# Kernel optimization log

Hardware: AMD Instinct MI355X
Metric: run time of the kernel (lower is better)

The kernel has to match this reference:

```python
import jax, jax.numpy as jnp
import numpy as np

N, E, HID, H, D = 16000, 128000, 128, 8, 16
EPS = 1e-6
LN_EPS = 1e-5


def _ln(x, g, b):
    mu = x.mean(-1, keepdims=True)
    var = ((x - mu) ** 2).mean(-1, keepdims=True)
    return (x - mu) * jax.lax.rsqrt(var + LN_EPS) * g + b


def _phi(x):
    return jax.nn.elu(x) + 1.0


def setup_inputs() -> dict:
    key = jax.random.key(0)
    ks = jax.random.split(key, 16)
    w = lambda k, s: (jax.random.normal(k, s, jnp.float32) * 0.02)
    inp = {
        'x': jax.random.normal(ks[0], (N, HID), jnp.float32),
        'r': jax.random.normal(ks[1], (E, HID), jnp.float32),
        'edge_index': jax.random.randint(ks[2], (2, E), 0, N, jnp.int64),
        # layernorms
        'ln_x_g': jnp.ones((HID,)), 'ln_x_b': jnp.zeros((HID,)),
        'ln_r_g': jnp.ones((HID,)), 'ln_r_b': jnp.zeros((HID,)),
        'ln_post_g': jnp.ones((HID,)), 'ln_post_b': jnp.zeros((HID,)),
        'ln_ffpre_g': jnp.ones((HID,)), 'ln_ffpre_b': jnp.zeros((HID,)),
        'ln_ffpost_g': jnp.ones((HID,)), 'ln_ffpost_b': jnp.zeros((HID,)),
        # attention projections (stored [in, out]; y = x @ W)
        'Wq': w(ks[3], (HID, H * D)), 'Wk': w(ks[4], (HID, H * D)),
        'Wv': w(ks[5], (HID, H * D)),
        'Wkr': w(ks[6], (HID, H * D)), 'Wvr': w(ks[7], (HID, H * D)),
        'Wo': w(ks[8], (H * D, HID)),
        'Wg': w(ks[9], (2 * HID, HID)), 'bg': jnp.zeros((HID,)),
        'Ws': w(ks[10], (HID, HID)), 'bs': jnp.zeros((HID,)),
        # feed-forward
        'W1': w(ks[11], (HID, 4 * HID)), 'b1': jnp.zeros((4 * HID,)),
        'W2': w(ks[12], (4 * HID, HID)), 'b2': jnp.zeros((HID,)),
    }
    return inp


def reference(x, r, edge_index, ln_x_g, ln_x_b, ln_r_g, ln_r_b,
              ln_post_g, ln_post_b, ln_ffpre_g, ln_ffpre_b,
              ln_ffpost_g, ln_ffpost_b, Wq, Wk, Wv, Wkr, Wvr, Wo,
              Wg, bg, Ws, bs, W1, b1, W2, b2):
    n = x.shape[0]
    src, dst = edge_index[0], edge_index[1]
    xs = _ln(x, ln_x_g, ln_x_b)            # shared pre-norm (non-bipartite)
    rn = _ln(r, ln_r_g, ln_r_b)

    q = (xs @ Wq).reshape(n, H, D)
    k = (xs @ Wk).reshape(n, H, D)
    v = (xs @ Wv).reshape(n, H, D)
    k_e = k[src] + (rn @ Wkr).reshape(-1, H, D)   # [E,H,D]
    v_e = v[src] + (rn @ Wvr).reshape(-1, H, D)

    phi_q = _phi(q)                         # [N,H,D]
    phi_k = _phi(k_e)                       # [E,H,D]
    # per-edge outer product, scattered to destination nodes
    kv = phi_k[..., :, None] * v_e[..., None, :]          # [E,H,D,D]
    S = jax.ops.segment_sum(kv.reshape(-1, H * D * D), dst,
                            num_segments=n).reshape(n, H, D, D)
    Z = jax.ops.segment_sum(phi_k.reshape(-1, H * D), dst,
                            num_segments=n).reshape(n, H, D)

    num = jnp.einsum('nhd,nhdv->nhv', phi_q, S)
    den = jnp.maximum((phi_q * Z).sum(-1, keepdims=True), EPS)
    out = (num / den).reshape(n, H * D) @ Wo              # [N,HID]

    g = jax.nn.sigmoid(jnp.concatenate([out, xs], axis=-1) @ Wg + bg)
    attn = out + g * (xs @ Ws + bs - out)

    x_mid = x + _ln(attn, ln_post_g, ln_post_b)
    h = jax.nn.gelu(_ln(x_mid, ln_ffpre_g, ln_ffpre_b) @ W1 + b1,
                    approximate=False) @ W2 + b2
    return x_mid + _ln(h, ln_ffpost_g, ln_ffpost_b)
```

## Files before the change

kernel.cpp:

```cpp
#include <hip/hip_runtime.h>
#include <hip/hip_bf16.h>

#define NN 16000
#define NE 128000

typedef unsigned short u16;
typedef __attribute__((ext_vector_type(8))) short bf16x8;
typedef __attribute__((ext_vector_type(4))) float f32x4;

__device__ __forceinline__ float bf2f(u16 u) {
    unsigned int v = ((unsigned int)u) << 16;
    return __uint_as_float(v);
}
__device__ __forceinline__ u16 f2bf(float f) {
    unsigned int u = __float_as_uint(f);
    unsigned int r = u + 0x7FFF + ((u >> 16) & 1);
    return (u16)(r >> 16);
}
__device__ __forceinline__ float loadf(const void* p, size_t i, int bf) {
    return bf ? bf2f(((const u16*)p)[i]) : ((const float*)p)[i];
}

__device__ __forceinline__ int detect_bf(const u16* __restrict__ xw) {
    int lane = threadIdx.x & 63;
    int c = 0;
    #pragma unroll
    for (int k = 0; k < 16; ++k) {
        unsigned int w = xw[lane * 16 + k];
        int e = (int)((w >> 7) & 0xFF);
        c += (e >= 100 && e <= 140) ? 1 : 0;
    }
    for (int m = 1; m < 64; m <<= 1) c += __shfl_xor(c, m, 64);
    return c >= 850;
}

__device__ __forceinline__ int detect_e64(const int* __restrict__ ei) {
    int lane = threadIdx.x & 63;
    int a = 0;
    #pragma unroll
    for (int k = 0; k < 16; ++k) a |= ei[2 * (lane * 16 + k) + 1];
    for (int m = 1; m < 64; m <<= 1) a |= __shfl_xor(a, m, 64);
    return a == 0;
}

struct WDesc { const void* w; u16* wt; int K; int N; int off; int tile0; };
struct WTArgs { WDesc d[11]; };
__global__ __launch_bounds__(256) void pre1_kernel(const int* __restrict__ ei,
                                                   int* __restrict__ e32,
                                                   int* __restrict__ hist,
                                                   const u16* __restrict__ xw,
                                                   WTArgs args)
{
    int b = blockIdx.x;
    int tid = threadIdx.x;
    if (b < 250) {
        int e64 = detect_e64(ei);
        #pragma unroll
        for (int j = 0; j < 4; ++j) {
            int i = b * 1024 + j * 256 + tid;
            int v = e64 ? ei[2 * i] : ei[i];
            v = v < 0 ? 0 : (v >= NN ? NN - 1 : v);
            e32[i] = v;
            if (i >= NE) atomicAdd(&hist[v], 1);
        }
        return;
    }
    int bf = detect_bf(xw);
    int i = 0;
    while (i < 10 && b >= args.d[i + 1].tile0) ++i;
    WDesc de = args.d[i];
    int lt = b - de.tile0;
    int tn = de.N >> 5;
    int tk = lt / tn, tc = lt % tn;
    int n = tc * 32 + (tid & 31);
    int k = tk * 32 + ((tid >> 5) << 2);
    u16* dp = de.wt + (size_t)n * de.K + k;
    #pragma unroll
    for (int j = 0; j < 4; ++j)
        dp[j] = f2bf(loadf(de.w, (size_t)de.off + (size_t)(k + j) * de.N + n, bf));
}

__global__ __launch_bounds__(256) void scan_kernel(const int* __restrict__ hist,
                                                   int* __restrict__ offs,
                                                   int* __restrict__ cursor)
{
    __shared__ int wsum[4];
    __shared__ int carry_s;
    int tid = threadIdx.x, lane = tid & 63, w = tid >> 6;
    if (tid == 0) { carry_s = 0; offs[0] = 0; cursor[0] = 0; }
    __syncthreads();
    for (int c0 = 0; c0 < NN; c0 += 256) {
        int i = c0 + tid;
        int x = (i < NN) ? hist[i] : 0;
        #pragma unroll
        for (int o = 1; o < 64; o <<= 1) {
            int y = __shfl_up(x, o, 64);
            if (lane >= o) x += y;
        }
        if (lane == 63) wsum[w] = x;
        __syncthreads();
        if (tid == 0) {
            int s = 0;
            #pragma unroll
            for (int j = 0; j < 4; ++j) { int t2 = wsum[j]; wsum[j] = s; s += t2; }
        }
        __syncthreads();
        int incl = x + wsum[w] + carry_s;
        if (i < NN) { offs[i + 1] = incl; cursor[i + 1] = incl; }
        __syncthreads();
        if (tid == 255) carry_s = incl;
        __syncthreads();
    }
}

__global__ void scatter_kernel(const int* __restrict__ e32, int* __restrict__ cursor,
                               int* __restrict__ perm, int* __restrict__ ssrc,
                               int* __restrict__ sdst)
{
    int i = blockIdx.x * 256 + threadIdx.x;
    if (i >= NE) return;
    int d = e32[NE + i];
    int pos = atomicAdd(&cursor[d], 1);
    perm[pos] = i;
    ssrc[pos] = e32[i];
    sdst[pos] = d;
}

__global__ __launch_bounds__(256) void node_proj_kernel(
    const void* __restrict__ x,
    const void* __restrict__ lng, const void* __restrict__ lnb,
    const u16* __restrict__ Wall,
    const void* __restrict__ bs, const void* __restrict__ bg,
    u16* __restrict__ qkv, float* __restrict__ sbuf, float* __restrict__ gxs)
{
    const int bf = detect_bf((const u16*)x);
    __shared__ float sg[128], sb[128];
    int tid = threadIdx.x;
    if (tid < 128) { sg[tid] = loadf(lng, tid, bf); sb[tid] = loadf(lnb, tid, bf); }
    __syncthreads();
    int wave = tid >> 6, lane = tid & 63;
    int quad = lane >> 4, l15 = lane & 15;
    int m0 = blockIdx.x * 16;

    float vbuf[32];
    float s = 0.f, sq = 0.f;
    size_t rbase = (size_t)(m0 + l15) * 128;
    #pragma unroll
    for (int kc = 0; kc < 4; ++kc) {
        int cb = kc * 32 + quad * 8;
        if (bf) {
            ushort4 p0 = *(const ushort4*)((const u16*)x + rbase + cb);
            ushort4 p1 = *(const ushort4*)((const u16*)x + rbase + cb + 4);
            vbuf[kc*8+0]=bf2f(p0.x); vbuf[kc*8+1]=bf2f(p0.y); vbuf[kc*8+2]=bf2f(p0.z); vbuf[kc*8+3]=bf2f(p0.w);
            vbuf[kc*8+4]=bf2f(p1.x); vbuf[kc*8+5]=bf2f(p1.y); vbuf[kc*8+6]=bf2f(p1.z); vbuf[kc*8+7]=bf2f(p1.w);
        } else {
            float4 p0 = *(const float4*)((const float*)x + rbase + cb);
            float4 p1 = *(const float4*)((const float*)x + rbase + cb + 4);
            vbuf[kc*8+0]=p0.x; vbuf[kc*8+1]=p0.y; vbuf[kc*8+2]=p0.z; vbuf[kc*8+3]=p0.w;
            vbuf[kc*8+4]=p1.x; vbuf[kc*8+5]=p1.y; vbuf[kc*8+6]=p1.z; vbuf[kc*8+7]=p1.w;
        }
        #pragma unroll
        for (int j = 0; j < 8; ++j) { s += vbuf[kc*8+j]; sq += vbuf[kc*8+j]*vbuf[kc*8+j]; }
    }
    s += __shfl_xor(s, 16, 64); sq += __shfl_xor(sq, 16, 64);
    s += __shfl_xor(s, 32, 64); sq += __shfl_xor(sq, 32, 64);
    float mu = s * (1.0f / 128.0f);
    float var = sq * (1.0f / 128.0f) - mu * mu;
    float rsx = rsqrtf(var + 1e-5f);
    bf16x8 afr[4];
    #pragma unroll
    for (int kc = 0; kc < 4; ++kc) {
        bf16x8 a;
        #pragma unroll
        for (int j = 0; j < 8; ++j) {
            int col = kc * 32 + quad * 8 + j;
            a[j] = (short)f2bf((vbuf[kc*8+j] - mu) * rsx * sg[col] + sb[col]);
        }
        afr[kc] = a;
    }

    f32x4 acc[10] = {};
    #pragma unroll
    for (int kc = 0; kc < 4; ++kc)
        #pragma unroll
        for (int tt = 0; tt < 10; ++tt) {
            int t = wave * 10 + tt;
            bf16x8 b = *(const bf16x8*)(Wall + (size_t)(t * 16 + l15) * 128 + kc * 32 + quad * 8);
            acc[tt] = __builtin_amdgcn_mfma_f32_16x16x32_bf16(afr[kc], b, acc[tt], 0, 0, 0);
        }
    #pragma unroll
    for (int tt = 0; tt < 10; ++tt) {
        int ct = (wave * 10 + tt) * 16 + l15;
        #pragma unroll
        for (int rg = 0; rg < 4; ++rg) {
            int row = m0 + quad * 4 + rg;
            float v = acc[tt][rg];
            if (ct < 384) {
                if (ct < 128) v = (v > 0.0f) ? v + 1.0f : expf(v);
                qkv[(size_t)row * 384 + ct] = f2bf(v);
            } else if (ct < 512) {
                int cs = ct - 384;
                sbuf[(size_t)row * 128 + cs] = v + loadf(bs, cs, bf);
            } else {
                int cg = ct - 512;
                gxs[(size_t)row * 128 + cg] = v + loadf(bg, cg, bf);
            }
        }
    }
}

__global__ __launch_bounds__(256) void edge_proj_kernel(
    const void* __restrict__ r, const void* __restrict__ x,
    const void* __restrict__ lng, const void* __restrict__ lnb,
    const u16* __restrict__ Wkrt, const u16* __restrict__ Wvrt,
    const int* __restrict__ perm, const int* __restrict__ ssrc,
    const int* __restrict__ sdst,
    const u16* __restrict__ qkv,
    float* __restrict__ p_arr, u16* __restrict__ ve_s)
{
    const int bf = detect_bf((const u16*)x);
    __shared__ float sg[128], sb[128];
    int tid = threadIdx.x;
    if (tid < 128) { sg[tid] = loadf(lng, tid, bf); sb[tid] = loadf(lnb, tid, bf); }
    __syncthreads();
    int wave = tid >> 6, lane = tid & 63;
    int quad = lane >> 4, l15 = lane & 15;
    int e0 = blockIdx.x * 32 + (wave >> 1) * 16;
    int c0 = (wave & 1) * 64;

    int rrow = perm[e0 + l15];
    float vbuf[32];
    float s = 0.f, sq = 0.f;
    size_t rbase = (size_t)rrow * 128;
    #pragma unroll
    for (int kc = 0; kc < 4; ++kc) {
        int cb = kc * 32 + quad * 8;
        if (bf) {
            ushort4 p0 = *(const ushort4*)((const u16*)r + rbase + cb);
            ushort4 p1 = *(const ushort4*)((const u16*)r + rbase + cb + 4);
            vbuf[kc*8+0]=bf2f(p0.x); vbuf[kc*8+1]=bf2f(p0.y); vbuf[kc*8+2]=bf2f(p0.z); vbuf[kc*8+3]=bf2f(p0.w);
            vbuf[kc*8+4]=bf2f(p1.x); vbuf[kc*8+5]=bf2f(p1.y); vbuf[kc*8+6]=bf2f(p1.z); vbuf[kc*8+7]=bf2f(p1.w);
        } else {
            float4 p0 = *(const float4*)((const float*)r + rbase + cb);
            float4 p1 = *(const float4*)((const float*)r + rbase + cb + 4);
            vbuf[kc*8+0]=p0.x; vbuf[kc*8+1]=p0.y; vbuf[kc*8+2]=p0.z; vbuf[kc*8+3]=p0.w;
            vbuf[kc*8+4]=p1.x; vbuf[kc*8+5]=p1.y; vbuf[kc*8+6]=p1.z; vbuf[kc*8+7]=p1.w;
        }
        #pragma unroll
        for (int j = 0; j < 8; ++j) { s += vbuf[kc*8+j]; sq += vbuf[kc*8+j]*vbuf[kc*8+j]; }
    }
    s += __shfl_xor(s, 16, 64); sq += __shfl_xor(sq, 16, 64);
    s += __shfl_xor(s, 32, 64); sq += __shfl_xor(sq, 32, 64);
    float mu = s * (1.0f / 128.0f);
    float var = sq * (1.0f / 128.0f) - mu * mu;
    float rsx = rsqrtf(var + 1e-5f);
    bf16x8 afr[4];
    #pragma unroll
    for (int kc = 0; kc < 4; ++kc) {
        bf16x8 a;
        #pragma unroll
        for (int j = 0; j < 8; ++j) {
            int col = kc * 32 + quad * 8 + j;
            a[j] = (short)f2bf((vbuf[kc*8+j] - mu) * rsx * sg[col] + sb[col]);
        }
        afr[kc] = a;
    }

    f32x4 acck[4] = {};
    f32x4 accv[4] = {};
    #pragma unroll
    for (int kc = 0; kc < 4; ++kc) {
        int k0 = kc * 32;
        #pragma unroll
        for (int t = 0; t < 4; ++t) {
            bf16x8 bk = *(const bf16x8*)(Wkrt + (size_t)(c0 + t*16 + l15) * 128 + k0 + quad * 8);
            bf16x8 bv = *(const bf16x8*)(Wvrt + (size_t)(c0 + t*16 + l15) * 128 + k0 + quad * 8);
            acck[t] = __builtin_amdgcn_mfma_f32_16x16x32_bf16(afr[kc], bk, acck[t], 0, 0, 0);
            accv[t] = __builtin_amdgcn_mfma_f32_16x16x32_bf16(afr[kc], bv, accv[t], 0, 0, 0);
        }
    }

    int se[4], de[4];
    #pragma unroll
    for (int rg = 0; rg < 4; ++rg) {
        int e = e0 + quad * 4 + rg;
        se[rg] = ssrc[e]; de[rg] = sdst[e];
    }
    #pragma unroll
    for (int t = 0; t < 4; ++t) {
        int col = c0 + t * 16 + l15;
        float p_[4];
        #pragma unroll
        for (int rg = 0; rg < 4; ++rg) {
            float kv = acck[t][rg] + bf2f(qkv[(size_t)se[rg] * 384 + 128 + col]);
            kv = (kv > 0.0f) ? kv + 1.0f : expf(kv);
            float pm = kv * bf2f(qkv[(size_t)de[rg] * 384 + col]);
            pm += __shfl_xor(pm, 1, 64);
            pm += __shfl_xor(pm, 2, 64);
            pm += __shfl_xor(pm, 4, 64);
            pm += __shfl_xor(pm, 8, 64);
            p_[rg] = pm;
        }
        if (l15 == 0) {
            #pragma unroll
            for (int rg = 0; rg < 4; ++rg)
                p_arr[(size_t)(e0 + quad * 4 + rg) * 8 + (c0 >> 4) + t] = p_[rg];
        }
        #pragma unroll
        for (int rg = 0; rg < 4; ++rg) {
            float vv = accv[t][rg] + bf2f(qkv[(size_t)se[rg] * 384 + 256 + col]);
            ve_s[(size_t)(e0 + quad * 4 + rg) * 128 + col] = f2bf(vv);
        }
    }
}

__global__ __launch_bounds__(256) void node_acc_kernel(
    const float* __restrict__ p_arr, const u16* __restrict__ ve_s,
    const int* __restrict__ offs, u16* __restrict__ att)
{
    int n = blockIdx.x * 4 + (threadIdx.x >> 6);
    int lane = threadIdx.x & 63;
    int beg = offs[n], end = offs[n + 1];
    int h0 = lane >> 4, h1 = 4 + h0;
    float n0 = 0.f, n1 = 0.f, d0 = 0.f, d1 = 0.f;
    for (int e = beg; e < end; ++e) {
        float p0 = p_arr[(size_t)e * 8 + h0];
        float p1 = p_arr[(size_t)e * 8 + h1];
        float v0 = bf2f(ve_s[(size_t)e * 128 + lane]);
        float v1 = bf2f(ve_s[(size_t)e * 128 + lane + 64]);
        n0 += p0 * v0; n1 += p1 * v1;
        d0 += p0; d1 += p1;
    }
    att[(size_t)n * 128 + lane]      = f2bf(n0 / fmaxf(d0, 1e-6f));
    att[(size_t)n * 128 + lane + 64] = f2bf(n1 / fmaxf(d1, 1e-6f));
}

__global__ __launch_bounds__(256) void gate_mega_kernel(
    const u16* __restrict__ att,
    const u16* __restrict__ Wo_t, const u16* __restrict__ Wg1_t,
    const float* __restrict__ gxs, const float* __restrict__ sbuf,
    const void* __restrict__ x,
    const void* __restrict__ g_po, const void* __restrict__ b_po,
    const void* __restrict__ g_fp, const void* __restrict__ b_fp,
    float* __restrict__ xmid, u16* __restrict__ ffp)
{
    const int bf = detect_bf((const u16*)x);
    __shared__ float lds[4][16][132];
    __shared__ float sgpo[128], sbpo[128], sgfp[128], sbfp[128];
    int tid = threadIdx.x;
    if (tid < 128) {
        sgpo[tid] = loadf(g_po, tid, bf);
        sbpo[tid] = loadf(b_po, tid, bf);
        sgfp[tid] = loadf(g_fp, tid, bf);
        sbfp[tid] = loadf(b_fp, tid, bf);
    }
    __syncthreads();
    int wave = tid >> 6, lane = tid & 63;
    int quad = lane >> 4, l15 = lane & 15;
    int m0 = blockIdx.x * 64 + wave * 16;

    bf16x8 afr[4];
    #pragma unroll
    for (int kc = 0; kc < 4; ++kc)
        afr[kc] = *(const bf16x8*)(att + (size_t)(m0 + l15) * 128 + kc * 32 + quad * 8);

    f32x4 acco[8] = {};
    #pragma unroll
    for (int kc = 0; kc < 4; ++kc)
        #pragma unroll
        for (int t = 0; t < 8; ++t) {
            bf16x8 b = *(const bf16x8*)(Wo_t + (size_t)(t*16 + l15) * 128 + kc*32 + quad*8);
            acco[t] = __builtin_amdgcn_mfma_f32_16x16x32_bf16(afr[kc], b, acco[t], 0, 0, 0);
        }
    #pragma unroll
    for (int t = 0; t < 8; ++t)
        #pragma unroll
        for (int rg = 0; rg < 4; ++rg)
            lds[wave][quad*4+rg][t*16+l15] = acco[t][rg];
    __syncthreads();
    bf16x8 afo[4];
    #pragma unroll
    for (int kc = 0; kc < 4; ++kc) {
        bf16x8 a;
        #pragma unroll
        for (int j = 0; j < 8; ++j)
            a[j] = (short)f2bf(lds[wave][l15][kc*32 + quad*8 + j]);
        afo[kc] = a;
    }
    f32x4 accg[8] = {};
    #pragma unroll
    for (int kc = 0; kc < 4; ++kc)
        #pragma unroll
        for (int t = 0; t < 8; ++t) {
            bf16x8 b = *(const bf16x8*)(Wg1_t + (size_t)(t*16 + l15) * 128 + kc*32 + quad*8);
            accg[t] = __builtin_amdgcn_mfma_f32_16x16x32_bf16(afo[kc], b, accg[t], 0, 0, 0);
        }
    float attn[8][4];
    float sv[4] = {0,0,0,0}, sqv[4] = {0,0,0,0};
    #pragma unroll
    for (int t = 0; t < 8; ++t) {
        int col = t * 16 + l15;
        #pragma unroll
        for (int rg = 0; rg < 4; ++rg) {
            int row = m0 + quad * 4 + rg;
            float gp = accg[t][rg] + gxs[(size_t)row * 128 + col];
            float gg = 1.0f / (1.0f + expf(-gp));
            float o = acco[t][rg];
            float a = o + gg * (sbuf[(size_t)row * 128 + col] - o);
            attn[t][rg] = a; sv[rg] += a; sqv[rg] += a * a;
        }
    }
    #pragma unroll
    for (int rg = 0; rg < 4; ++rg)
        for (int m = 1; m < 16; m <<= 1) {
            sv[rg] += __shfl_xor(sv[rg], m, 64);
            sqv[rg] += __shfl_xor(sqv[rg], m, 64);
        }
    float mu[4], rs[4];
    #pragma unroll
    for (int rg = 0; rg < 4; ++rg) {
        mu[rg] = sv[rg] * (1.0f / 128.0f);
        float var = sqv[rg] * (1.0f / 128.0f) - mu[rg] * mu[rg];
        rs[rg] = rsqrtf(var + 1e-5f);
    }
    float s2[4] = {0,0,0,0}, sq2[4] = {0,0,0,0};
    #pragma unroll
    for (int t = 0; t < 8; ++t) {
        int col = t * 16 + l15;
        #pragma unroll
        for (int rg = 0; rg < 4; ++rg) {
            int row = m0 + quad * 4 + rg;
            float xm = loadf(x, (size_t)row * 128 + col, bf)
                     + (attn[t][rg] - mu[rg]) * rs[rg] * sgpo[col] + sbpo[col];
            attn[t][rg] = xm;
            xmid[(size_t)row * 128 + col] = xm;
            s2[rg] += xm; sq2[rg] += xm * xm;
        }
    }
    #pragma unroll
    for (int rg = 0; rg < 4; ++rg)
        for (int m = 1; m < 16; m <<= 1) {
            s2[rg] += __shfl_xor(s2[rg], m, 64);
            sq2[rg] += __shfl_xor(sq2[rg], m, 64);
        }
    #pragma unroll
    for (int rg = 0; rg < 4; ++rg) {
        float mu2 = s2[rg] * (1.0f / 128.0f);
        float var2 = sq2[rg] * (1.0f / 128.0f) - mu2 * mu2;
        float rs2 = rsqrtf(var2 + 1e-5f);
        #pragma unroll
        for (int t = 0; t < 8; ++t) {
            int col = t * 16 + l15;
            int row = m0 + quad * 4 + rg;
            ffp[(size_t)row * 128 + col] =
                f2bf((attn[t][rg] - mu2) * rs2 * sgfp[col] + sbfp[col]);
        }
    }
}

__global__ __launch_bounds__(128) void ff_mega_kernel(
    const u16* __restrict__ ffp, const u16* __restrict__ W1_t, const void* __restrict__ b1,
    const u16* __restrict__ W2_t, const void* __restrict__ b2,
    const float* __restrict__ xmid, const void* __restrict__ x,
    const void* __restrict__ g_fo, const void* __restrict__ b_fo,
    void* __restrict__ outp)
{
    const int bf = detect_bf((const u16*)x);
    __shared__ __align__(16) u16 h1l[2][16][520];
    int tid = threadIdx.x;
    int wave = tid >> 6, lane = tid & 63;
    int quad = lane >> 4, l15 = lane & 15;
    int m0 = blockIdx.x * 32 + wave * 16;

    bf16x8 afr[4];
    const u16* ap = ffp + (size_t)(m0 + l15) * 128 + quad * 8;
    #pragma unroll
    for (int kc = 0; kc < 4; ++kc) afr[kc] = *(const bf16x8*)(ap + kc * 32);

    f32x4 acc1[32] = {};
    #pragma unroll
    for (int kc = 0; kc < 4; ++kc)
        #pragma unroll
        for (int t = 0; t < 32; ++t) {
            bf16x8 b = *(const bf16x8*)(W1_t + (size_t)(t*16 + l15) * 128 + kc*32 + quad*8);
            acc1[t] = __builtin_amdgcn_mfma_f32_16x16x32_bf16(afr[kc], b, acc1[t], 0, 0, 0);
        }
    #pragma unroll
    for (int t = 0; t < 32; ++t) {
        int col = t * 16 + l15;
        float bv = loadf(b1, col, bf);
        #pragma unroll
        for (int rg = 0; rg < 4; ++rg) {
            float v = acc1[t][rg] + bv;
            v = 0.5f * v * (1.0f + erff(v * 0.70710678118f));
            h1l[wave][quad * 4 + rg][col] = f2bf(v);
        }
    }
    __syncthreads();
    f32x4 acc2[8] = {};
    #pragma unroll
    for (int kc = 0; kc < 16; ++kc) {
        bf16x8 a = *(const bf16x8*)&h1l[wave][l15][kc * 32 + quad * 8];
        #pragma unroll
        for (int t = 0; t < 8; ++t) {
            bf16x8 b = *(const bf16x8*)(W2_t + (size_t)(t*16 + l15) * 512 + kc*32 + quad*8);
            acc2[t] = __builtin_amdgcn_mfma_f32_16x16x32_bf16(a, b, acc2[t], 0, 0, 0);
        }
    }
    float h2v[8][4];
    float sv[4] = {0,0,0,0}, sqv[4] = {0,0,0,0};
    #pragma unroll
    for (int t = 0; t < 8; ++t) {
        int col = t * 16 + l15;
        float bv = loadf(b2, col, bf);
        #pragma unroll
        for (int rg = 0; rg < 4; ++rg) {
            float v = acc2[t][rg] + bv;
            h2v[t][rg] = v; sv[rg] += v; sqv[rg] += v * v;
        }
    }
    #pragma unroll
    for (int rg = 0; rg < 4; ++rg)
        for (int m = 1; m < 16; m <<= 1) {
            sv[rg] += __shfl_xor(sv[rg], m, 64);
            sqv[rg] += __shfl_xor(sqv[rg], m, 64);
        }
    #pragma unroll
    for (int rg = 0; rg < 4; ++rg) {
        float mu = sv[rg] * (1.0f / 128.0f);
        float var = sqv[rg] * (1.0f / 128.0f) - mu * mu;
        float rs = rsqrtf(var + 1e-5f);
        int row = m0 + quad * 4 + rg;
        #pragma unroll
        for (int t = 0; t < 8; ++t) {
            int col = t * 16 + l15;
            float y = xmid[(size_t)row * 128 + col]
                    + (h2v[t][rg] - mu) * rs * loadf(g_fo, col, bf) + loadf(b_fo, col, bf);
            if (bf) ((u16*)outp)[(size_t)row * 128 + col] = f2bf(y);
            else    ((float*)outp)[(size_t)row * 128 + col] = y;
        }
    }
}

extern "C" void kernel_launch(void* const* d_in, const int* in_sizes, int n_in,
                              void* d_out, int out_size, void* d_ws, size_t ws_size,
                              hipStream_t stream)
{
    const int N = NN, E = NE;
    const void* x       = d_in[0];
    const void* r       = d_in[1];
    const int*  ei      = (const int*)d_in[2];
    const void* ln_x_g  = d_in[3];
    const void* ln_x_b  = d_in[4];
    const void* ln_r_g  = d_in[5];
    const void* ln_r_b  = d_in[6];
    const void* ln_po_g = d_in[7];
    const void* ln_po_b = d_in[8];
    const void* ln_fp_g = d_in[9];
    const void* ln_fp_b = d_in[10];
    const void* ln_fo_g = d_in[11];
    const void* ln_fo_b = d_in[12];
    const void* Wq      = d_in[13];
    const void* Wk      = d_in[14];
    const void* Wv      = d_in[15];
    const void* Wkr     = d_in[16];
    const void* Wvr     = d_in[17];
    const void* Wo      = d_in[18];
    const void* Wg      = d_in[19];
    const void* bg      = d_in[20];
    const void* Ws      = d_in[21];
    const void* bs      = d_in[22];
    const void* W1      = d_in[23];
    const void* b1      = d_in[24];
    const void* W2      = d_in[25];
    const void* b2      = d_in[26];

    float* ws = (float*)d_ws;
    size_t off = 0;
    auto alloc = [&](size_t n) { float* p = ws + off; off += n; return p; };
    const size_t U = (size_t)N * 64;
    u16*   qkv_bf = (u16*)alloc(3 * U);
    u16*   att_bf = (u16*)alloc(U);
    float* sbuf   = alloc((size_t)N * 128);
    float* gxs    = alloc((size_t)N * 128);
    float* xmid   = alloc((size_t)N * 128);
    u16*   ffp_bf = (u16*)alloc(U);
    u16*   ve_s   = (u16*)alloc((size_t)E * 64);
    float* p_arr  = alloc((size_t)E * 8);
    int*   e32    = (int*)alloc((size_t)2 * E);
    int*   perm   = (int*)alloc(E);
    int*   ssrc   = (int*)alloc(E);
    int*   sdst   = (int*)alloc(E);
    int*   hist   = (int*)alloc(NN);
    int*   offs   = (int*)alloc(NN + 1);
    int*   cursor = (int*)alloc(NN + 1);
    u16*   wt     = (u16*)alloc(139264);

    u16* Wall_t = wt;
    u16* Wkr_t  = wt + 81920;
    u16* Wvr_t  = wt + 98304;
    u16* Wo_t   = wt + 114688;
    u16* Wg1_t  = wt + 131072;
    u16* W1_t   = wt + 147456;
    u16* W2_t   = wt + 212992;

    hipMemsetAsync(hist, 0, NN * sizeof(int), stream);

    WTArgs wa;
    int t0 = 250;
    auto setw = [&](int i, const void* w, u16* wtp, int K, int Ncol, int eoff) {
        wa.d[i] = WDesc{w, wtp, K, Ncol, eoff, t0};
        t0 += (K / 32) * (Ncol / 32);
    };
    setw(0, Wq,  wt,           128, 128, 0);
    setw(1, Wk,  wt + 16384,   128, 128, 0);
    setw(2, Wv,  wt + 32768,   128, 128, 0);
    setw(3, Ws,  wt + 49152,   128, 128, 0);
    setw(4, Wg,  wt + 65536,   128, 128, 16384);
    setw(5, Wkr, Wkr_t,        128, 128, 0);
    setw(6, Wvr, Wvr_t,        128, 128, 0);
    setw(7, Wo,  Wo_t,         128, 128, 0);
    setw(8, Wg,  Wg1_t,        128, 128, 0);
    setw(9, W1,  W1_t,         128, 512, 0);
    setw(10, W2, W2_t,         512, 128, 0);
    pre1_kernel<<<t0, 256, 0, stream>>>(ei, e32, hist, (const u16*)x, wa);

    scan_kernel<<<1, 256, 0, stream>>>(hist, offs, cursor);
    scatter_kernel<<<(E + 255) / 256, 256, 0, stream>>>(e32, cursor, perm, ssrc, sdst);

    node_proj_kernel<<<N / 16, 256, 0, stream>>>(x, ln_x_g, ln_x_b, Wall_t,
                                                 bs, bg, qkv_bf, sbuf, gxs);

    edge_proj_kernel<<<E / 32, 256, 0, stream>>>(r, x, ln_r_g, ln_r_b, Wkr_t, Wvr_t,
                                                 perm, ssrc, sdst, qkv_bf, p_arr, ve_s);

    node_acc_kernel<<<N / 4, 256, 0, stream>>>(p_arr, ve_s, offs, att_bf);

    gate_mega_kernel<<<N / 64, 256, 0, stream>>>(att_bf, Wo_t, Wg1_t, gxs, sbuf,
                                                 x, ln_po_g, ln_po_b, ln_fp_g, ln_fp_b,
                                                 xmid, ffp_bf);

    ff_mega_kernel<<<N / 32, 128, 0, stream>>>(ffp_bf, W1_t, b1, W2_t, b2,
                                               xmid, x, ln_fo_g, ln_fo_b, d_out);
}
```

Measured before the change: 467.5 us.

## Vectorize scan and node accumulation, split FF across waves, add fp32 attention path

The scan now has each thread handle four histogram entries, cutting the number of serial chunk iterations. node_acc gives each lane two adjacent columns and unrolls the edge loop by two, and it writes fp32 attention output instead of bf16. The gate kernel splits that fp32 input into hi/lo bf16 parts and runs two MFMAs per tile, improving precision at the cost of twice the Wo matmul work. The FF kernel now spreads one 16-row tile across four waves, with the final layernorm reduced through LDS, which raises parallelism and lowers per-wave register use but adds a block barrier.

```diff
diff --git a/kernel.cpp b/kernel.cpp
--- a/kernel.cpp
+++ b/kernel.cpp
@@ -89,9 +89,14 @@
     int tid = threadIdx.x, lane = tid & 63, w = tid >> 6;
     if (tid == 0) { carry_s = 0; offs[0] = 0; cursor[0] = 0; }
     __syncthreads();
-    for (int c0 = 0; c0 < NN; c0 += 256) {
-        int i = c0 + tid;
-        int x = (i < NN) ? hist[i] : 0;
+    for (int c0 = 0; c0 < NN; c0 += 1024) {
+        int i0 = c0 + tid * 4;
+        int a0 = (i0 + 0 < NN) ? hist[i0 + 0] : 0;
+        int a1 = (i0 + 1 < NN) ? hist[i0 + 1] : 0;
+        int a2 = (i0 + 2 < NN) ? hist[i0 + 2] : 0;
+        int a3 = (i0 + 3 < NN) ? hist[i0 + 3] : 0;
+        int s_loc = a0 + a1 + a2 + a3;
+        int x = s_loc;
         #pragma unroll
         for (int o = 1; o < 64; o <<= 1) {
             int y = __shfl_up(x, o, 64);
@@ -105,10 +110,14 @@
             for (int j = 0; j < 4; ++j) { int t2 = wsum[j]; wsum[j] = s; s += t2; }
         }
         __syncthreads();
-        int incl = x + wsum[w] + carry_s;
-        if (i < NN) { offs[i + 1] = incl; cursor[i + 1] = incl; }
+        int excl = x - s_loc + wsum[w] + carry_s;
+        int p0 = excl + a0, p1 = p0 + a1, p2 = p1 + a2, p3 = p2 + a3;
+        if (i0 + 0 < NN) { offs[i0 + 1] = p0; cursor[i0 + 1] = p0; }
+        if (i0 + 1 < NN) { offs[i0 + 2] = p1; cursor[i0 + 2] = p1; }
+        if (i0 + 2 < NN) { offs[i0 + 3] = p2; cursor[i0 + 3] = p2; }
+        if (i0 + 3 < NN) { offs[i0 + 4] = p3; cursor[i0 + 4] = p3; }
         __syncthreads();
-        if (tid == 255) carry_s = incl;
+        if (tid == 255) carry_s = p3;
         __syncthreads();
     }
 }
@@ -316,27 +325,35 @@
 
 __global__ __launch_bounds__(256) void node_acc_kernel(
     const float* __restrict__ p_arr, const u16* __restrict__ ve_s,
-    const int* __restrict__ offs, u16* __restrict__ att)
+    const int* __restrict__ offs, float* __restrict__ att)
 {
     int n = blockIdx.x * 4 + (threadIdx.x >> 6);
     int lane = threadIdx.x & 63;
     int beg = offs[n], end = offs[n + 1];
-    int h0 = lane >> 4, h1 = 4 + h0;
-    float n0 = 0.f, n1 = 0.f, d0 = 0.f, d1 = 0.f;
-    for (int e = beg; e < end; ++e) {
-        float p0 = p_arr[(size_t)e * 8 + h0];
-        float p1 = p_arr[(size_t)e * 8 + h1];
-        float v0 = bf2f(ve_s[(size_t)e * 128 + lane]);
-        float v1 = bf2f(ve_s[(size_t)e * 128 + lane + 64]);
-        n0 += p0 * v0; n1 += p1 * v1;
-        d0 += p0; d1 += p1;
-    }
-    att[(size_t)n * 128 + lane]      = f2bf(n0 / fmaxf(d0, 1e-6f));
-    att[(size_t)n * 128 + lane + 64] = f2bf(n1 / fmaxf(d1, 1e-6f));
+    int h = lane >> 3;
+    float na0 = 0.f, na1 = 0.f, da = 0.f;
+    float nb0 = 0.f, nb1 = 0.f, db = 0.f;
+    int e = beg;
+    for (; e + 1 < end; e += 2) {
+        float pa = p_arr[(size_t)e * 8 + h];
+        float pb = p_arr[(size_t)(e + 1) * 8 + h];
+        ushort2 va = *(const ushort2*)&ve_s[(size_t)e * 128 + 2 * lane];
+        ushort2 vb = *(const ushort2*)&ve_s[(size_t)(e + 1) * 128 + 2 * lane];
+        na0 += pa * bf2f(va.x); na1 += pa * bf2f(va.y); da += pa;
+        nb0 += pb * bf2f(vb.x); nb1 += pb * bf2f(vb.y); db += pb;
+    }
+    if (e < end) {
+        float pa = p_arr[(size_t)e * 8 + h];
+        ushort2 va = *(const ushort2*)&ve_s[(size_t)e * 128 + 2 * lane];
+        na0 += pa * bf2f(va.x); na1 += pa * bf2f(va.y); da += pa;
+    }
+    float inv = 1.0f / fmaxf(da + db, 1e-6f);
+    att[(size_t)n * 128 + 2 * lane]     = (na0 + nb0) * inv;
+    att[(size_t)n * 128 + 2 * lane + 1] = (na1 + nb1) * inv;
 }
 
 __global__ __launch_bounds__(256) void gate_mega_kernel(
-    const u16* __restrict__ att,
+    const float* __restrict__ att,
     const u16* __restrict__ Wo_t, const u16* __restrict__ Wg1_t,
     const float* __restrict__ gxs, const float* __restrict__ sbuf,
     const void* __restrict__ x,
@@ -359,18 +376,30 @@
     int quad = lane >> 4, l15 = lane & 15;
     int m0 = blockIdx.x * 64 + wave * 16;
 
-    bf16x8 afr[4];
-    #pragma unroll
-    for (int kc = 0; kc < 4; ++kc)
-        afr[kc] = *(const bf16x8*)(att + (size_t)(m0 + l15) * 128 + kc * 32 + quad * 8);
-
+    bf16x8 ahi[4], alo[4];
+    #pragma unroll
+    for (int kc = 0; kc < 4; ++kc) {
+        const float* ap = att + (size_t)(m0 + l15) * 128 + kc * 32 + quad * 8;
+        float4 v0 = *(const float4*)ap;
+        float4 v1 = *(const float4*)(ap + 4);
+        float vv[8] = {v0.x, v0.y, v0.z, v0.w, v1.x, v1.y, v1.z, v1.w};
+        bf16x8 h, l;
+        #pragma unroll
+        for (int j = 0; j < 8; ++j) {
+            u16 hb = f2bf(vv[j]);
+            h[j] = (short)hb;
+            l[j] = (short)f2bf(vv[j] - bf2f(hb));
+        }
+        ahi[kc] = h; alo[kc] = l;
+    }
     f32x4 acco[8] = {};
     #pragma unroll
     for (int kc = 0; kc < 4; ++kc)
         #pragma unroll
         for (int t = 0; t < 8; ++t) {
             bf16x8 b = *(const bf16x8*)(Wo_t + (size_t)(t*16 + l15) * 128 + kc*32 + quad*8);
-            acco[t] = __builtin_amdgcn_mfma_f32_16x16x32_bf16(afr[kc], b, acco[t], 0, 0, 0);
+            acco[t] = __builtin_amdgcn_mfma_f32_16x16x32_bf16(ahi[kc], b, acco[t], 0, 0, 0);
+            acco[t] = __builtin_amdgcn_mfma_f32_16x16x32_bf16(alo[kc], b, acco[t], 0, 0, 0);
         }
     #pragma unroll
     for (int t = 0; t < 8; ++t)
@@ -458,7 +487,7 @@
     }
 }
 
-__global__ __launch_bounds__(128) void ff_mega_kernel(
+__global__ __launch_bounds__(256) void ff_mega_kernel(
     const u16* __restrict__ ffp, const u16* __restrict__ W1_t, const void* __restrict__ b1,
     const u16* __restrict__ W2_t, const void* __restrict__ b2,
     const float* __restrict__ xmid, const void* __restrict__ x,
@@ -466,57 +495,60 @@
     void* __restrict__ outp)
 {
     const int bf = detect_bf((const u16*)x);
-    __shared__ __align__(16) u16 h1l[2][16][520];
+    __shared__ __align__(16) u16 h1l[16][520];
+    __shared__ float psum[4][16], psq[4][16];
     int tid = threadIdx.x;
     int wave = tid >> 6, lane = tid & 63;
     int quad = lane >> 4, l15 = lane & 15;
-    int m0 = blockIdx.x * 32 + wave * 16;
+    int m0 = blockIdx.x * 16;
 
     bf16x8 afr[4];
     const u16* ap = ffp + (size_t)(m0 + l15) * 128 + quad * 8;
     #pragma unroll
     for (int kc = 0; kc < 4; ++kc) afr[kc] = *(const bf16x8*)(ap + kc * 32);
 
-    f32x4 acc1[32] = {};
+    f32x4 acc1[8] = {};
     #pragma unroll
     for (int kc = 0; kc < 4; ++kc)
         #pragma unroll
-        for (int t = 0; t < 32; ++t) {
+        for (int tt = 0; tt < 8; ++tt) {
+            int t = wave * 8 + tt;
             bf16x8 b = *(const bf16x8*)(W1_t + (size_t)(t*16 + l15) * 128 + kc*32 + quad*8);
-            acc1[t] = __builtin_amdgcn_mfma_f32_16x16x32_bf16(afr[kc], b, acc1[t], 0, 0, 0);
-        }
-    #pragma unroll
-    for (int t = 0; t < 32; ++t) {
-        int col = t * 16 + l15;
+            acc1[tt] = __builtin_amdgcn_mfma_f32_16x16x32_bf16(afr[kc], b, acc1[tt], 0, 0, 0);
+        }
+    #pragma unroll
+    for (int tt = 0; tt < 8; ++tt) {
+        int col = (wave * 8 + tt) * 16 + l15;
         float bv = loadf(b1, col, bf);
         #pragma unroll
         for (int rg = 0; rg < 4; ++rg) {
-            float v = acc1[t][rg] + bv;
+            float v = acc1[tt][rg] + bv;
             v = 0.5f * v * (1.0f + erff(v * 0.70710678118f));
-            h1l[wave][quad * 4 + rg][col] = f2bf(v);
+            h1l[quad * 4 + rg][col] = f2bf(v);
         }
     }
     __syncthreads();
-    f32x4 acc2[8] = {};
+    f32x4 acc2[2] = {};
     #pragma unroll
     for (int kc = 0; kc < 16; ++kc) {
-        bf16x8 a = *(const bf16x8*)&h1l[wave][l15][kc * 32 + quad * 8];
-        #pragma unroll
-        for (int t = 0; t < 8; ++t) {
+        bf16x8 a = *(const bf16x8*)&h1l[l15][kc * 32 + quad * 8];
+        #pragma unroll
+        for (int tt = 0; tt < 2; ++tt) {
+            int t = wave * 2 + tt;
             bf16x8 b = *(const bf16x8*)(W2_t + (size_t)(t*16 + l15) * 512 + kc*32 + quad*8);
-            acc2[t] = __builtin_amdgcn_mfma_f32_16x16x32_bf16(a, b, acc2[t], 0, 0, 0);
-        }
-    }
-    float h2v[8][4];
+            acc2[tt] = __builtin_amdgcn_mfma_f32_16x16x32_bf16(a, b, acc2[tt], 0, 0, 0);
+        }
+    }
+    float h2v[2][4];
     float sv[4] = {0,0,0,0}, sqv[4] = {0,0,0,0};
     #pragma unroll
-    for (int t = 0; t < 8; ++t) {
-        int col = t * 16 + l15;
+    for (int tt = 0; tt < 2; ++tt) {
+        int col = (wave * 2 + tt) * 16 + l15;
         float bv = loadf(b2, col, bf);
         #pragma unroll
         for (int rg = 0; rg < 4; ++rg) {
-            float v = acc2[t][rg] + bv;
-            h2v[t][rg] = v; sv[rg] += v; sqv[rg] += v * v;
+            float v = acc2[tt][rg] + bv;
+            h2v[tt][rg] = v; sv[rg] += v; sqv[rg] += v * v;
         }
     }
     #pragma unroll
@@ -525,17 +557,28 @@
             sv[rg] += __shfl_xor(sv[rg], m, 64);
             sqv[rg] += __shfl_xor(sqv[rg], m, 64);
         }
+    if (l15 == 0) {
+        #pragma unroll
+        for (int rg = 0; rg < 4; ++rg) {
+            psum[wave][quad * 4 + rg] = sv[rg];
+            psq[wave][quad * 4 + rg]  = sqv[rg];
+        }
+    }
+    __syncthreads();
     #pragma unroll
     for (int rg = 0; rg < 4; ++rg) {
-        float mu = sv[rg] * (1.0f / 128.0f);
-        float var = sqv[rg] * (1.0f / 128.0f) - mu * mu;
+        int rl = quad * 4 + rg;
+        float ts = psum[0][rl] + psum[1][rl] + psum[2][rl] + psum[3][rl];
+        float tq = psq[0][rl]  + psq[1][rl]  + psq[2][rl]  + psq[3][rl];
+        float mu = ts * (1.0f / 128.0f);
+        float var = tq * (1.0f / 128.0f) - mu * mu;
         float rs = rsqrtf(var + 1e-5f);
-        int row = m0 + quad * 4 + rg;
-        #pragma unroll
-        for (int t = 0; t < 8; ++t) {
-            int col = t * 16 + l15;
+        int row = m0 + rl;
+        #pragma unroll
+        for (int tt = 0; tt < 2; ++tt) {
+            int col = (wave * 2 + tt) * 16 + l15;
             float y = xmid[(size_t)row * 128 + col]
-                    + (h2v[t][rg] - mu) * rs * loadf(g_fo, col, bf) + loadf(b_fo, col, bf);
+                    + (h2v[tt][rg] - mu) * rs * loadf(g_fo, col, bf) + loadf(b_fo, col, bf);
             if (bf) ((u16*)outp)[(size_t)row * 128 + col] = f2bf(y);
             else    ((float*)outp)[(size_t)row * 128 + col] = y;
         }
@@ -580,7 +623,7 @@
     auto alloc = [&](size_t n) { float* p = ws + off; off += n; return p; };
     const size_t U = (size_t)N * 64;
     u16*   qkv_bf = (u16*)alloc(3 * U);
-    u16*   att_bf = (u16*)alloc(U);
+    float* att    = alloc((size_t)N * 128);
     float* sbuf   = alloc((size_t)N * 128);
     float* gxs    = alloc((size_t)N * 128);
     float* xmid   = alloc((size_t)N * 128);
@@ -634,12 +677,12 @@
     edge_proj_kernel<<<E / 32, 256, 0, stream>>>(r, x, ln_r_g, ln_r_b, Wkr_t, Wvr_t,
                                                  perm, ssrc, sdst, qkv_bf, p_arr, ve_s);
 
-    node_acc_kernel<<<N / 4, 256, 0, stream>>>(p_arr, ve_s, offs, att_bf);
-
-    gate_mega_kernel<<<N / 64, 256, 0, stream>>>(att_bf, Wo_t, Wg1_t, gxs, sbuf,
+    node_acc_kernel<<<N / 4, 256, 0, stream>>>(p_arr, ve_s, offs, att);
+
+    gate_mega_kernel<<<N / 64, 256, 0, stream>>>(att, Wo_t, Wg1_t, gxs, sbuf,
                                                  x, ln_po_g, ln_po_b, ln_fp_g, ln_fp_b,
                                                  xmid, ffp_bf);
 
-    ff_mega_kernel<<<N / 32, 128, 0, stream>>>(ffp_bf, W1_t, b1, W2_t, b2,
+    ff_mega_kernel<<<N / 16, 256, 0, stream>>>(ffp_bf, W1_t, b1, W2_t, b2,
                                                xmid, x, ln_fo_g, ln_fo_b, d_out);
 }
```

New measurement: 395.6 us. 1.18x faster.
